# Kernel tuning notes

Hardware: AMD Instinct MI355X
Metric: run time of the kernel (lower is better)

## Reference

```python
import jax, jax.numpy as jnp
import numpy as np

INPUT_DIM = 4096
BATCH = 64
E_PER = 262144  # edges per graph
MIN_SP = 0.3


def setup_inputs() -> dict:
    key = jax.random.key(0)
    k1, k2, k3 = jax.random.split(key, 3)
    E = BATCH * E_PER
    edge_index = jax.random.randint(k1, (2, E), 0, INPUT_DIM, dtype=jnp.int64)
    edge_attr = jax.random.normal(k2, (E,), dtype=jnp.float32)
    ptr = jnp.arange(BATCH + 1, dtype=jnp.int64)
    # learned parameter (xavier-normal-ish init)
    std = float(np.sqrt(2.0 / (INPUT_DIM + INPUT_DIM)))
    weight_mask = jax.random.normal(k3, (INPUT_DIM, INPUT_DIM), dtype=jnp.float32) * std
    return {"edge_index": edge_index, "edge_attr": edge_attr, "ptr": ptr, "weight_mask": weight_mask}


def reference(edge_index, edge_attr, ptr, weight_mask):
    B = ptr.shape[0] - 1
    E = edge_index.shape[1]
    e_per = E // B
    # symmetric sigmoid mask (dropout is None -> identity)
    sym = jax.nn.sigmoid(weight_mask.T + weight_mask)
    # x_reshape: [B, e_per]
    x = edge_attr.reshape(B, e_per)
    # edge_ind_reshape: [B, 2, e_per]
    ei = edge_index.T.reshape(B, e_per, 2).transpose(0, 2, 1)
    # gather mask weights for batch-0 edges
    src = ei[0, 0]
    dst = ei[0, 1]
    w = sym[src, dst]  # [e_per]
    num_rm = int(e_per * MIN_SP)  # static count of pruned edges
    order = jnp.argsort(w)
    pruned = order[:num_rm]
    kept = jnp.sort(order[num_rm:])  # boolean-mask compaction preserves order
    mask = jnp.ones((e_per,), dtype=bool).at[pruned].set(False)
    # filtered edge_index: [B, 2, K] -> permute(1,0,2) -> [2, B*K]
    fei = jnp.take(ei, kept, axis=2)
    out_edge_index = fei.transpose(1, 0, 2).reshape(2, -1)
    # filtered edge_attr: [B, K] -> [B*K]
    out_edge_attr = jnp.take(x, kept, axis=1).reshape(-1)
    return out_edge_index, out_edge_attr, mask
```

## Files before the change

kernel.cpp:

```cpp
#include <hip/hip_runtime.h>
#include <stdint.h>
#include <math.h>

#define TIECAP 4096
typedef unsigned long long ull;

struct Ctrl {
  ull prefix;
  int rank_rem;
  int tie_count;
  int num_rm;
};

__device__ __forceinline__ ull dkey(double d) {
  ull u = (ull)__double_as_longlong(d);
  return (u & 0x8000000000000000ull) ? ~u : (u | 0x8000000000000000ull);
}

__global__ void k_init(unsigned int* hist8, Ctrl* ctrl, int num_rm) {
  int t = blockIdx.x * blockDim.x + threadIdx.x;
  if (t < 8 * 256) hist8[t] = 0u;
  if (t == 0) {
    ctrl->prefix = 0ull;
    ctrl->rank_rem = num_rm - 1;
    ctrl->tie_count = 0;
    ctrl->num_rm = num_rm;
  }
}

__global__ void k_keys(const int* __restrict__ ei, const float* __restrict__ wm,
                       int N, long long E, int D,
                       ull* __restrict__ keys, unsigned int* __restrict__ hist0) {
  __shared__ unsigned int sh[256];
  if (threadIdx.x < 256) sh[threadIdx.x] = 0u;
  __syncthreads();
  int e = blockIdx.x * blockDim.x + threadIdx.x;
  if (e < N) {
    int src = ei[e];
    int dst = ei[E + e];
    double s = (double)wm[(long long)src * D + dst] + (double)wm[(long long)dst * D + src];
    ull k = dkey(s);
    keys[e] = k;
    atomicAdd(&sh[(unsigned int)(k >> 56)], 1u);
  }
  __syncthreads();
  if (threadIdx.x < 256 && sh[threadIdx.x]) atomicAdd(&hist0[threadIdx.x], sh[threadIdx.x]);
}

__global__ void k_hist(const ull* __restrict__ keys, int N, int level,
                       const Ctrl* __restrict__ ctrl, unsigned int* __restrict__ hist) {
  __shared__ unsigned int sh[256];
  if (threadIdx.x < 256) sh[threadIdx.x] = 0u;
  __syncthreads();
  int e = blockIdx.x * blockDim.x + threadIdx.x;
  int shift = 56 - 8 * level;
  if (e < N) {
    ull k = keys[e];
    ull prefix = ctrl->prefix;
    if (((k ^ prefix) >> (shift + 8)) == 0ull)
      atomicAdd(&sh[(unsigned int)(k >> shift) & 0xFFu], 1u);
  }
  __syncthreads();
  if (threadIdx.x < 256 && sh[threadIdx.x]) atomicAdd(&hist[threadIdx.x], sh[threadIdx.x]);
}

__global__ void k_pick(const unsigned int* __restrict__ hist, int level, Ctrl* ctrl) {
  __shared__ unsigned int sh[256];
  int t = threadIdx.x;
  unsigned int c = hist[t];
  sh[t] = c;
  __syncthreads();
  for (int off = 1; off < 256; off <<= 1) {
    unsigned int v = sh[t];
    unsigned int a = (t >= off) ? sh[t - off] : 0u;
    __syncthreads();
    sh[t] = v + a;
    __syncthreads();
  }
  unsigned int incl = sh[t];
  unsigned int excl = incl - c;
  unsigned int r = (unsigned int)ctrl->rank_rem;
  if (r >= excl && r < incl) {
    int shift = 56 - 8 * level;
    ctrl->prefix |= ((ull)t) << shift;
    ctrl->rank_rem = (int)(r - excl);
  }
}

__global__ void k_ties(const ull* __restrict__ keys, int N, Ctrl* ctrl,
                       int* __restrict__ tieIdx) {
  int e = blockIdx.x * blockDim.x + threadIdx.x;
  if (e >= N) return;
  if (keys[e] == ctrl->prefix) {
    int p = atomicAdd(&ctrl->tie_count, 1);
    if (p < TIECAP) tieIdx[p] = e;
  }
}

__device__ __forceinline__ bool is_kept(ull k, int e, ull T, int j, int tc,
                                        const int* __restrict__ tieIdx) {
  if (k < T) return false;
  if (k > T) return true;
  if (j <= 0) return true;
  if (tc > TIECAP) tc = TIECAP;
  int rank = 0;
  for (int i = 0; i < tc; ++i) rank += (tieIdx[i] < e) ? 1 : 0;
  return rank >= j;
}

__global__ void k_scanA(const ull* __restrict__ keys, int N,
                        const Ctrl* __restrict__ ctrl, const int* __restrict__ tieIdx,
                        int* __restrict__ pos, int* __restrict__ blockSums,
                        float* __restrict__ mask_out) {
  __shared__ int sh[1024];
  ull T = ctrl->prefix;
  int j = ctrl->rank_rem + 1;
  int tc = ctrl->tie_count;
  int e = blockIdx.x * 1024 + threadIdx.x;
  int m = 0;
  if (e < N) m = is_kept(keys[e], e, T, j, tc, tieIdx) ? 1 : 0;
  sh[threadIdx.x] = m;
  __syncthreads();
  for (int off = 1; off < 1024; off <<= 1) {
    int v = sh[threadIdx.x];
    int add = (threadIdx.x >= (unsigned)off) ? sh[threadIdx.x - off] : 0;
    __syncthreads();
    sh[threadIdx.x] = v + add;
    __syncthreads();
  }
  if (e < N) {
    pos[e] = ((sh[threadIdx.x] - m) << 1) | m;
    mask_out[e] = m ? 1.0f : 0.0f;
  }
  if (threadIdx.x == 1023) blockSums[blockIdx.x] = sh[1023];
}

__global__ void k_scanB(int* bs, int nb) {
  __shared__ int sh[256];
  int t = threadIdx.x;
  int v = (t < nb) ? bs[t] : 0;
  sh[t] = v;
  __syncthreads();
  for (int off = 1; off < 256; off <<= 1) {
    int x = sh[t];
    int a = (t >= off) ? sh[t - off] : 0;
    __syncthreads();
    sh[t] = x + a;
    __syncthreads();
  }
  if (t < nb) bs[t] = sh[t] - v;
}

__global__ void k_kidx(const int* __restrict__ pos, const int* __restrict__ blockSums,
                       int N, int* __restrict__ kidx) {
  int e = blockIdx.x * blockDim.x + threadIdx.x;
  if (e >= N) return;
  int p = pos[e];
  if (p & 1) kidx[(p >> 1) + blockSums[e >> 10]] = e;
}

__global__ void k_gather(const int* __restrict__ kidx, const int* __restrict__ ei,
                         const float* __restrict__ attr, long long E, int N,
                         int Kkeep, long long BK, long long total4,
                         float* __restrict__ out) {
  long long q = (long long)blockIdx.x * blockDim.x + threadIdx.x;
  if (q >= total4) return;
  long long f = q * 4;
  int row = (f >= 2 * BK) ? 2 : ((f >= BK) ? 1 : 0);
  int rb = (int)(f - (long long)row * BK);
  int b = rb / Kkeep;
  int kk = rb - b * Kkeep;
  long long colbase = (long long)b * N;
  if (kk + 4 <= Kkeep) {
    int i0 = kidx[kk], i1 = kidx[kk + 1], i2 = kidx[kk + 2], i3 = kidx[kk + 3];
    float4 v;
    if (row == 0) {
      v.x = (float)ei[colbase + i0]; v.y = (float)ei[colbase + i1];
      v.z = (float)ei[colbase + i2]; v.w = (float)ei[colbase + i3];
    } else if (row == 1) {
      const int* p = ei + E;
      v.x = (float)p[colbase + i0]; v.y = (float)p[colbase + i1];
      v.z = (float)p[colbase + i2]; v.w = (float)p[colbase + i3];
    } else {
      v.x = attr[colbase + i0]; v.y = attr[colbase + i1];
      v.z = attr[colbase + i2]; v.w = attr[colbase + i3];
    }
    *(float4*)(out + f) = v;
  } else {
    for (int i = 0; i < 4; ++i) {
      long long ff = f + i;
      int row2 = (ff >= 2 * BK) ? 2 : ((ff >= BK) ? 1 : 0);
      int rb2 = (int)(ff - (long long)row2 * BK);
      int b2 = rb2 / Kkeep;
      int kk2 = rb2 - b2 * Kkeep;
      int id = kidx[kk2];
      long long c = (long long)b2 * N + id;
      float v = (row2 == 0) ? (float)ei[c] : (row2 == 1) ? (float)ei[E + c] : attr[c];
      out[ff] = v;
    }
  }
}

extern "C" void kernel_launch(void* const* d_in, const int* in_sizes, int n_in,
                              void* d_out, int out_size, void* d_ws, size_t ws_size,
                              hipStream_t stream) {
  const int* ei = (const int*)d_in[0];
  const float* attr = (const float*)d_in[1];
  const float* wm = (const float*)d_in[3];

  int B = in_sizes[2] - 1;
  long long E = (long long)in_sizes[0] / 2;
  int e_per = (int)(E / B);
  int D = (int)llround(sqrt((double)in_sizes[3]));
  int num_rm = (int)((double)e_per * 0.3);
  int Kkeep = e_per - num_rm;
  long long BK = (long long)B * Kkeep;
  long long total4 = 3 * BK / 4;

  char* w = (char*)d_ws;
  size_t off = 0;
  ull* keys = (ull*)(w + off);            off += (size_t)e_per * 8;
  unsigned int* hist8 = (unsigned int*)(w + off); off += 8 * 256 * 4;
  int* pos = (int*)(w + off);             off += (size_t)e_per * 4;
  int nb = (e_per + 1023) / 1024;
  int* blockSums = (int*)(w + off);       off += (size_t)nb * 4;
  int* tieIdx = (int*)(w + off);          off += (size_t)TIECAP * 4;
  int* kidx = (int*)(w + off);            off += (size_t)Kkeep * 4;
  Ctrl* ctrl = (Ctrl*)(w + off);          off += sizeof(Ctrl);
  (void)ws_size; (void)n_in; (void)out_size;

  float* out = (float*)d_out;
  float* mask_out = out + 3 * BK;

  k_init<<<dim3(2), dim3(1024), 0, stream>>>(hist8, ctrl, num_rm);
  k_keys<<<dim3(nb), dim3(1024), 0, stream>>>(ei, wm, e_per, E, D, keys, hist8);
  k_pick<<<dim3(1), dim3(256), 0, stream>>>(hist8, 0, ctrl);
  for (int l = 1; l < 8; ++l) {
    k_hist<<<dim3(nb), dim3(1024), 0, stream>>>(keys, e_per, l, ctrl, hist8 + l * 256);
    k_pick<<<dim3(1), dim3(256), 0, stream>>>(hist8 + l * 256, l, ctrl);
  }
  k_ties<<<dim3(nb), dim3(1024), 0, stream>>>(keys, e_per, ctrl, tieIdx);
  k_scanA<<<dim3(nb), dim3(1024), 0, stream>>>(keys, e_per, ctrl, tieIdx, pos, blockSums, mask_out);
  k_scanB<<<dim3(1), dim3(256), 0, stream>>>(blockSums, nb);
  k_kidx<<<dim3(nb), dim3(1024), 0, stream>>>(pos, blockSums, e_per, kidx);
  int gblocks = (int)((total4 + 255) / 256);
  k_gather<<<dim3(gblocks), dim3(256), 0, stream>>>(kidx, ei, attr, E, e_per, Kkeep, BK, total4, out);
}
```

Baseline: 135.8 us.

## Use 32-bit float keys for radix select, fuse pick into histogram, compact via LDS

Radix select now runs on 32-bit float keys in four 8-bit levels instead of 64-bit double keys in eight. The per-level pick kernel is folded into the histogram kernel through a last-block-done counter, which removes many small launches. Ties at the float threshold are broken by recomputing the exact double key and comparing it against a small tie list. The gather through kidx is replaced by a block-local compaction that does coalesced vector loads, stages kept values in LDS and writes them out contiguously. In exchange it depends on the tie count staying under the reduced cap, it recomputes random weight reads for threshold edges, and its int4 loads assume e_per is divisible by 1024.

```diff
diff --git a/kernel.cpp b/kernel.cpp
--- a/kernel.cpp
+++ b/kernel.cpp
@@ -2,123 +2,163 @@
 #include <stdint.h>
 #include <math.h>
 
-#define TIECAP 4096
+#define TIECAP 1024
 typedef unsigned long long ull;
+typedef long long ll;
 
 struct Ctrl {
-  ull prefix;
+  unsigned int prefix;
   int rank_rem;
   int tie_count;
-  int num_rm;
+  int done0, done1, done2, done3;
 };
 
+__device__ __forceinline__ unsigned int fkey(float f) {
+  unsigned int u = __float_as_uint(f);
+  return (u & 0x80000000u) ? ~u : (u | 0x80000000u);
+}
 __device__ __forceinline__ ull dkey(double d) {
   ull u = (ull)__double_as_longlong(d);
   return (u & 0x8000000000000000ull) ? ~u : (u | 0x8000000000000000ull);
 }
 
-__global__ void k_init(unsigned int* hist8, Ctrl* ctrl, int num_rm) {
-  int t = blockIdx.x * blockDim.x + threadIdx.x;
-  if (t < 8 * 256) hist8[t] = 0u;
+__global__ void k_init(unsigned int* hist, Ctrl* ctrl, int num_rm) {
+  int t = threadIdx.x;
+  if (t < 1024) hist[t] = 0u;
   if (t == 0) {
-    ctrl->prefix = 0ull;
+    ctrl->prefix = 0u;
     ctrl->rank_rem = num_rm - 1;
     ctrl->tie_count = 0;
-    ctrl->num_rm = num_rm;
+    ctrl->done0 = 0; ctrl->done1 = 0; ctrl->done2 = 0; ctrl->done3 = 0;
+  }
+}
+
+__device__ void do_pick(unsigned int* hist, int shift, Ctrl* ctrl) {
+  __shared__ unsigned int sph[256];
+  __shared__ int s_r;
+  int t = threadIdx.x;
+  if (t == 0) s_r = ctrl->rank_rem;
+  unsigned int c = 0;
+  if (t < 256) { c = atomicAdd(&hist[t], 0u); sph[t] = c; }
+  __syncthreads();
+  for (int off = 1; off < 256; off <<= 1) {
+    unsigned int v = 0, a = 0;
+    if (t < 256) { v = sph[t]; a = (t >= off) ? sph[t - off] : 0u; }
+    __syncthreads();
+    if (t < 256) sph[t] = v + a;
+    __syncthreads();
+  }
+  if (t < 256) {
+    unsigned int incl = sph[t], excl = incl - c;
+    unsigned int r = (unsigned int)s_r;
+    if (r >= excl && r < incl) {
+      ctrl->prefix |= ((unsigned int)t) << shift;
+      ctrl->rank_rem = (int)(r - excl);
+    }
   }
 }
 
 __global__ void k_keys(const int* __restrict__ ei, const float* __restrict__ wm,
-                       int N, long long E, int D,
-                       ull* __restrict__ keys, unsigned int* __restrict__ hist0) {
+                       int N, ll E, int D, unsigned int* __restrict__ key32,
+                       unsigned int* hist, Ctrl* ctrl) {
   __shared__ unsigned int sh[256];
-  if (threadIdx.x < 256) sh[threadIdx.x] = 0u;
-  __syncthreads();
-  int e = blockIdx.x * blockDim.x + threadIdx.x;
+  __shared__ int s_last;
+  int t = threadIdx.x;
+  if (t < 256) sh[t] = 0u;
+  __syncthreads();
+  int e = blockIdx.x * 1024 + t;
   if (e < N) {
-    int src = ei[e];
-    int dst = ei[E + e];
-    double s = (double)wm[(long long)src * D + dst] + (double)wm[(long long)dst * D + src];
-    ull k = dkey(s);
-    keys[e] = k;
-    atomicAdd(&sh[(unsigned int)(k >> 56)], 1u);
-  }
-  __syncthreads();
-  if (threadIdx.x < 256 && sh[threadIdx.x]) atomicAdd(&hist0[threadIdx.x], sh[threadIdx.x]);
-}
-
-__global__ void k_hist(const ull* __restrict__ keys, int N, int level,
-                       const Ctrl* __restrict__ ctrl, unsigned int* __restrict__ hist) {
+    int src = ei[e], dst = ei[E + e];
+    double s = (double)wm[(ll)src * D + dst] + (double)wm[(ll)dst * D + src];
+    unsigned int k = fkey((float)s);
+    key32[e] = k;
+    atomicAdd(&sh[k >> 24], 1u);
+  }
+  __syncthreads();
+  if (t < 256 && sh[t]) atomicAdd(&hist[t], sh[t]);
+  __threadfence();
+  __syncthreads();
+  if (t == 0) s_last = (atomicAdd(&ctrl->done0, 1) == (int)gridDim.x - 1) ? 1 : 0;
+  __syncthreads();
+  if (!s_last) return;
+  do_pick(hist, 24, ctrl);
+}
+
+__global__ void k_level(const unsigned int* __restrict__ key32, int N, int level,
+                        unsigned int* hist, Ctrl* ctrl, int* done) {
   __shared__ unsigned int sh[256];
-  if (threadIdx.x < 256) sh[threadIdx.x] = 0u;
-  __syncthreads();
-  int e = blockIdx.x * blockDim.x + threadIdx.x;
-  int shift = 56 - 8 * level;
+  __shared__ int s_last;
+  int t = threadIdx.x;
+  if (t < 256) sh[t] = 0u;
+  __syncthreads();
+  unsigned int prefix = ctrl->prefix;
+  int shift = 24 - 8 * level;
+  int e = blockIdx.x * 1024 + t;
   if (e < N) {
-    ull k = keys[e];
-    ull prefix = ctrl->prefix;
-    if (((k ^ prefix) >> (shift + 8)) == 0ull)
-      atomicAdd(&sh[(unsigned int)(k >> shift) & 0xFFu], 1u);
-  }
-  __syncthreads();
-  if (threadIdx.x < 256 && sh[threadIdx.x]) atomicAdd(&hist[threadIdx.x], sh[threadIdx.x]);
-}
-
-__global__ void k_pick(const unsigned int* __restrict__ hist, int level, Ctrl* ctrl) {
-  __shared__ unsigned int sh[256];
-  int t = threadIdx.x;
-  unsigned int c = hist[t];
-  sh[t] = c;
-  __syncthreads();
-  for (int off = 1; off < 256; off <<= 1) {
-    unsigned int v = sh[t];
-    unsigned int a = (t >= off) ? sh[t - off] : 0u;
-    __syncthreads();
-    sh[t] = v + a;
-    __syncthreads();
-  }
-  unsigned int incl = sh[t];
-  unsigned int excl = incl - c;
-  unsigned int r = (unsigned int)ctrl->rank_rem;
-  if (r >= excl && r < incl) {
-    int shift = 56 - 8 * level;
-    ctrl->prefix |= ((ull)t) << shift;
-    ctrl->rank_rem = (int)(r - excl);
-  }
-}
-
-__global__ void k_ties(const ull* __restrict__ keys, int N, Ctrl* ctrl,
-                       int* __restrict__ tieIdx) {
+    unsigned int k = key32[e];
+    if (((k ^ prefix) >> (shift + 8)) == 0u)
+      atomicAdd(&sh[(k >> shift) & 0xFFu], 1u);
+  }
+  __syncthreads();
+  if (t < 256 && sh[t]) atomicAdd(&hist[t], sh[t]);
+  __threadfence();
+  __syncthreads();
+  if (t == 0) s_last = (atomicAdd(done, 1) == (int)gridDim.x - 1) ? 1 : 0;
+  __syncthreads();
+  if (!s_last) return;
+  do_pick(hist, shift, ctrl);
+}
+
+__global__ void k_ties(const unsigned int* __restrict__ key32,
+                       const int* __restrict__ ei, const float* __restrict__ wm,
+                       int N, ll E, int D, Ctrl* ctrl,
+                       int* __restrict__ tieIdx, ull* __restrict__ tieKey) {
   int e = blockIdx.x * blockDim.x + threadIdx.x;
   if (e >= N) return;
-  if (keys[e] == ctrl->prefix) {
+  if (key32[e] == ctrl->prefix) {
     int p = atomicAdd(&ctrl->tie_count, 1);
-    if (p < TIECAP) tieIdx[p] = e;
-  }
-}
-
-__device__ __forceinline__ bool is_kept(ull k, int e, ull T, int j, int tc,
-                                        const int* __restrict__ tieIdx) {
+    if (p < TIECAP) {
+      int src = ei[e], dst = ei[E + e];
+      double s = (double)wm[(ll)src * D + dst] + (double)wm[(ll)dst * D + src];
+      tieIdx[p] = e;
+      tieKey[p] = dkey(s);
+    }
+  }
+}
+
+__device__ __forceinline__ bool is_kept(unsigned int k, int e, unsigned int T,
+                                        int j, int tc,
+                                        const int* __restrict__ tieIdx,
+                                        const ull* __restrict__ tieKey,
+                                        const int* __restrict__ ei,
+                                        const float* __restrict__ wm, ll E, int D) {
   if (k < T) return false;
   if (k > T) return true;
   if (j <= 0) return true;
   if (tc > TIECAP) tc = TIECAP;
+  int src = ei[e], dst = ei[E + e];
+  ull me = dkey((double)wm[(ll)src * D + dst] + (double)wm[(ll)dst * D + src]);
   int rank = 0;
-  for (int i = 0; i < tc; ++i) rank += (tieIdx[i] < e) ? 1 : 0;
+  for (int i = 0; i < tc; ++i) {
+    ull o = tieKey[i];
+    rank += (o < me || (o == me && tieIdx[i] < e)) ? 1 : 0;
+  }
   return rank >= j;
 }
 
-__global__ void k_scanA(const ull* __restrict__ keys, int N,
-                        const Ctrl* __restrict__ ctrl, const int* __restrict__ tieIdx,
-                        int* __restrict__ pos, int* __restrict__ blockSums,
-                        float* __restrict__ mask_out) {
+__global__ void k_scanA(const unsigned int* __restrict__ key32, int N,
+                        const Ctrl* __restrict__ ctrl,
+                        const int* __restrict__ tieIdx, const ull* __restrict__ tieKey,
+                        const int* __restrict__ ei, const float* __restrict__ wm,
+                        ll E, int D, int* __restrict__ pos,
+                        int* __restrict__ blockSums, float* __restrict__ mask_out) {
   __shared__ int sh[1024];
-  ull T = ctrl->prefix;
+  unsigned int T = ctrl->prefix;
   int j = ctrl->rank_rem + 1;
   int tc = ctrl->tie_count;
   int e = blockIdx.x * 1024 + threadIdx.x;
   int m = 0;
-  if (e < N) m = is_kept(keys[e], e, T, j, tc, tieIdx) ? 1 : 0;
+  if (e < N) m = is_kept(key32[e], e, T, j, tc, tieIdx, tieKey, ei, wm, E, D) ? 1 : 0;
   sh[threadIdx.x] = m;
   __syncthreads();
   for (int off = 1; off < 1024; off <<= 1) {
@@ -151,54 +191,37 @@
   if (t < nb) bs[t] = sh[t] - v;
 }
 
-__global__ void k_kidx(const int* __restrict__ pos, const int* __restrict__ blockSums,
-                       int N, int* __restrict__ kidx) {
-  int e = blockIdx.x * blockDim.x + threadIdx.x;
-  if (e >= N) return;
-  int p = pos[e];
-  if (p & 1) kidx[(p >> 1) + blockSums[e >> 10]] = e;
-}
-
-__global__ void k_gather(const int* __restrict__ kidx, const int* __restrict__ ei,
-                         const float* __restrict__ attr, long long E, int N,
-                         int Kkeep, long long BK, long long total4,
-                         float* __restrict__ out) {
-  long long q = (long long)blockIdx.x * blockDim.x + threadIdx.x;
-  if (q >= total4) return;
-  long long f = q * 4;
-  int row = (f >= 2 * BK) ? 2 : ((f >= BK) ? 1 : 0);
-  int rb = (int)(f - (long long)row * BK);
-  int b = rb / Kkeep;
-  int kk = rb - b * Kkeep;
-  long long colbase = (long long)b * N;
-  if (kk + 4 <= Kkeep) {
-    int i0 = kidx[kk], i1 = kidx[kk + 1], i2 = kidx[kk + 2], i3 = kidx[kk + 3];
-    float4 v;
-    if (row == 0) {
-      v.x = (float)ei[colbase + i0]; v.y = (float)ei[colbase + i1];
-      v.z = (float)ei[colbase + i2]; v.w = (float)ei[colbase + i3];
-    } else if (row == 1) {
-      const int* p = ei + E;
-      v.x = (float)p[colbase + i0]; v.y = (float)p[colbase + i1];
-      v.z = (float)p[colbase + i2]; v.w = (float)p[colbase + i3];
-    } else {
-      v.x = attr[colbase + i0]; v.y = attr[colbase + i1];
-      v.z = attr[colbase + i2]; v.w = attr[colbase + i3];
-    }
-    *(float4*)(out + f) = v;
+__global__ void k_compact(const int* __restrict__ pos, const int* __restrict__ bs,
+                          const int* __restrict__ ei, const float* __restrict__ attr,
+                          ll E, int N, int Kkeep, ll BK, float* __restrict__ out) {
+  __shared__ float lds[1024];
+  __shared__ int s_cnt;
+  int t = threadIdx.x;
+  int blk = blockIdx.x;
+  int b = blockIdx.y;
+  int r = blockIdx.z;
+  int q = blk * 256 + t;
+  int4 p4 = ((const int4*)pos)[q];
+  ll cb = (ll)b * N;
+  float4 v;
+  if (r == 0) {
+    int4 d = ((const int4*)(ei + cb))[q];
+    v = make_float4((float)d.x, (float)d.y, (float)d.z, (float)d.w);
+  } else if (r == 1) {
+    int4 d = ((const int4*)(ei + E + cb))[q];
+    v = make_float4((float)d.x, (float)d.y, (float)d.z, (float)d.w);
   } else {
-    for (int i = 0; i < 4; ++i) {
-      long long ff = f + i;
-      int row2 = (ff >= 2 * BK) ? 2 : ((ff >= BK) ? 1 : 0);
-      int rb2 = (int)(ff - (long long)row2 * BK);
-      int b2 = rb2 / Kkeep;
-      int kk2 = rb2 - b2 * Kkeep;
-      int id = kidx[kk2];
-      long long c = (long long)b2 * N + id;
-      float v = (row2 == 0) ? (float)ei[c] : (row2 == 1) ? (float)ei[E + c] : attr[c];
-      out[ff] = v;
-    }
-  }
+    v = ((const float4*)(attr + cb))[q];
+  }
+  if (p4.x & 1) lds[p4.x >> 1] = v.x;
+  if (p4.y & 1) lds[p4.y >> 1] = v.y;
+  if (p4.z & 1) lds[p4.z >> 1] = v.z;
+  if (p4.w & 1) lds[p4.w >> 1] = v.w;
+  if (t == 255) s_cnt = (p4.w >> 1) + (p4.w & 1);
+  __syncthreads();
+  ll ob = (ll)r * BK + (ll)b * Kkeep + bs[blk];
+  int cnt = s_cnt;
+  for (int i = t; i < cnt; i += 256) out[ob + i] = lds[i];
 }
 
 extern "C" void kernel_launch(void* const* d_in, const int* in_sizes, int n_in,
@@ -209,40 +232,37 @@
   const float* wm = (const float*)d_in[3];
 
   int B = in_sizes[2] - 1;
-  long long E = (long long)in_sizes[0] / 2;
+  ll E = (ll)in_sizes[0] / 2;
   int e_per = (int)(E / B);
   int D = (int)llround(sqrt((double)in_sizes[3]));
   int num_rm = (int)((double)e_per * 0.3);
   int Kkeep = e_per - num_rm;
-  long long BK = (long long)B * Kkeep;
-  long long total4 = 3 * BK / 4;
+  ll BK = (ll)B * Kkeep;
+  int nb = (e_per + 1023) / 1024;
 
   char* w = (char*)d_ws;
   size_t off = 0;
-  ull* keys = (ull*)(w + off);            off += (size_t)e_per * 8;
-  unsigned int* hist8 = (unsigned int*)(w + off); off += 8 * 256 * 4;
-  int* pos = (int*)(w + off);             off += (size_t)e_per * 4;
-  int nb = (e_per + 1023) / 1024;
-  int* blockSums = (int*)(w + off);       off += (size_t)nb * 4;
-  int* tieIdx = (int*)(w + off);          off += (size_t)TIECAP * 4;
-  int* kidx = (int*)(w + off);            off += (size_t)Kkeep * 4;
-  Ctrl* ctrl = (Ctrl*)(w + off);          off += sizeof(Ctrl);
+  unsigned int* key32 = (unsigned int*)(w + off); off += (size_t)e_per * 4;
+  int* pos = (int*)(w + off);                     off += (size_t)e_per * 4;
+  unsigned int* hist = (unsigned int*)(w + off);  off += 4 * 256 * 4;
+  int* blockSums = (int*)(w + off);               off += (size_t)nb * 4;
+  int* tieIdx = (int*)(w + off);                  off += (size_t)TIECAP * 4;
+  ull* tieKey = (ull*)(w + off);                  off += (size_t)TIECAP * 8;
+  Ctrl* ctrl = (Ctrl*)(w + off);                  off += sizeof(Ctrl);
   (void)ws_size; (void)n_in; (void)out_size;
 
   float* out = (float*)d_out;
   float* mask_out = out + 3 * BK;
 
-  k_init<<<dim3(2), dim3(1024), 0, stream>>>(hist8, ctrl, num_rm);
-  k_keys<<<dim3(nb), dim3(1024), 0, stream>>>(ei, wm, e_per, E, D, keys, hist8);
-  k_pick<<<dim3(1), dim3(256), 0, stream>>>(hist8, 0, ctrl);
-  for (int l = 1; l < 8; ++l) {
-    k_hist<<<dim3(nb), dim3(1024), 0, stream>>>(keys, e_per, l, ctrl, hist8 + l * 256);
-    k_pick<<<dim3(1), dim3(256), 0, stream>>>(hist8 + l * 256, l, ctrl);
-  }
-  k_ties<<<dim3(nb), dim3(1024), 0, stream>>>(keys, e_per, ctrl, tieIdx);
-  k_scanA<<<dim3(nb), dim3(1024), 0, stream>>>(keys, e_per, ctrl, tieIdx, pos, blockSums, mask_out);
+  k_init<<<dim3(1), dim3(1024), 0, stream>>>(hist, ctrl, num_rm);
+  k_keys<<<dim3(nb), dim3(1024), 0, stream>>>(ei, wm, e_per, E, D, key32, hist, ctrl);
+  k_level<<<dim3(nb), dim3(1024), 0, stream>>>(key32, e_per, 1, hist + 256, ctrl, &ctrl->done1);
+  k_level<<<dim3(nb), dim3(1024), 0, stream>>>(key32, e_per, 2, hist + 512, ctrl, &ctrl->done2);
+  k_level<<<dim3(nb), dim3(1024), 0, stream>>>(key32, e_per, 3, hist + 768, ctrl, &ctrl->done3);
+  k_ties<<<dim3(nb), dim3(1024), 0, stream>>>(key32, ei, wm, e_per, E, D, ctrl, tieIdx, tieKey);
+  k_scanA<<<dim3(nb), dim3(1024), 0, stream>>>(key32, e_per, ctrl, tieIdx, tieKey,
+                                               ei, wm, E, D, pos, blockSums, mask_out);
   k_scanB<<<dim3(1), dim3(256), 0, stream>>>(blockSums, nb);
-  k_kidx<<<dim3(nb), dim3(1024), 0, stream>>>(pos, blockSums, e_per, kidx);
-  int gblocks = (int)((total4 + 255) / 256);
-  k_gather<<<dim3(gblocks), dim3(256), 0, stream>>>(kidx, ei, attr, E, e_per, Kkeep, BK, total4, out);
-}
+  k_compact<<<dim3(nb, B, 3), dim3(256), 0, stream>>>(pos, blockSums, ei, attr,
+                                                      E, e_per, Kkeep, BK, out);
+}
```

Measured after the change: 343.1 us. +152.6%, slower.

## Replace 8-pass radix select with 16-bit histogram plus candidate rank and fused compaction

Applied to the files above, without the earlier changes.

Uses 32-bit float keys instead of 64-bit double keys. The threshold search becomes a single 65536-bin histogram, a pick pass, and a small candidate-set rank that folds ties in via an (key,index) packed comparison. This replaces eight histogram/pick launch pairs and the tie-rank loop. The separate pos/kidx/gather kernels are merged into one streaming compaction kernel that reads each batch's data contiguously and writes kept entries directly. The trade-offs are global atomics on the histogram and a cap on the candidate count. Float rounding of the key may also change the ordering relative to the double-precision reference.

```diff
diff --git a/kernel.cpp b/kernel.cpp
--- a/kernel.cpp
+++ b/kernel.cpp
@@ -2,137 +2,104 @@
 #include <stdint.h>
 #include <math.h>
 
-#define TIECAP 4096
+#define CAND_CAP 8192
 typedef unsigned long long ull;
+typedef long long ll;
+typedef unsigned int uint;
 
 struct Ctrl {
-  ull prefix;
-  int rank_rem;
-  int tie_count;
-  int num_rm;
+  int binsel;
+  int r_in;
+  int ncand;
+  int pad;
+  ull Tpack;
 };
 
-__device__ __forceinline__ ull dkey(double d) {
-  ull u = (ull)__double_as_longlong(d);
-  return (u & 0x8000000000000000ull) ? ~u : (u | 0x8000000000000000ull);
-}
-
-__global__ void k_init(unsigned int* hist8, Ctrl* ctrl, int num_rm) {
-  int t = blockIdx.x * blockDim.x + threadIdx.x;
-  if (t < 8 * 256) hist8[t] = 0u;
-  if (t == 0) {
-    ctrl->prefix = 0ull;
-    ctrl->rank_rem = num_rm - 1;
-    ctrl->tie_count = 0;
-    ctrl->num_rm = num_rm;
-  }
-}
-
 __global__ void k_keys(const int* __restrict__ ei, const float* __restrict__ wm,
-                       int N, long long E, int D,
-                       ull* __restrict__ keys, unsigned int* __restrict__ hist0) {
-  __shared__ unsigned int sh[256];
-  if (threadIdx.x < 256) sh[threadIdx.x] = 0u;
-  __syncthreads();
-  int e = blockIdx.x * blockDim.x + threadIdx.x;
-  if (e < N) {
-    int src = ei[e];
-    int dst = ei[E + e];
-    double s = (double)wm[(long long)src * D + dst] + (double)wm[(long long)dst * D + src];
-    ull k = dkey(s);
-    keys[e] = k;
-    atomicAdd(&sh[(unsigned int)(k >> 56)], 1u);
-  }
-  __syncthreads();
-  if (threadIdx.x < 256 && sh[threadIdx.x]) atomicAdd(&hist0[threadIdx.x], sh[threadIdx.x]);
-}
-
-__global__ void k_hist(const ull* __restrict__ keys, int N, int level,
-                       const Ctrl* __restrict__ ctrl, unsigned int* __restrict__ hist) {
-  __shared__ unsigned int sh[256];
-  if (threadIdx.x < 256) sh[threadIdx.x] = 0u;
-  __syncthreads();
-  int e = blockIdx.x * blockDim.x + threadIdx.x;
-  int shift = 56 - 8 * level;
-  if (e < N) {
-    ull k = keys[e];
-    ull prefix = ctrl->prefix;
-    if (((k ^ prefix) >> (shift + 8)) == 0ull)
-      atomicAdd(&sh[(unsigned int)(k >> shift) & 0xFFu], 1u);
-  }
-  __syncthreads();
-  if (threadIdx.x < 256 && sh[threadIdx.x]) atomicAdd(&hist[threadIdx.x], sh[threadIdx.x]);
-}
-
-__global__ void k_pick(const unsigned int* __restrict__ hist, int level, Ctrl* ctrl) {
-  __shared__ unsigned int sh[256];
-  int t = threadIdx.x;
-  unsigned int c = hist[t];
-  sh[t] = c;
-  __syncthreads();
-  for (int off = 1; off < 256; off <<= 1) {
-    unsigned int v = sh[t];
-    unsigned int a = (t >= off) ? sh[t - off] : 0u;
-    __syncthreads();
-    sh[t] = v + a;
-    __syncthreads();
-  }
-  unsigned int incl = sh[t];
-  unsigned int excl = incl - c;
-  unsigned int r = (unsigned int)ctrl->rank_rem;
-  if (r >= excl && r < incl) {
-    int shift = 56 - 8 * level;
-    ctrl->prefix |= ((ull)t) << shift;
-    ctrl->rank_rem = (int)(r - excl);
-  }
-}
-
-__global__ void k_ties(const ull* __restrict__ keys, int N, Ctrl* ctrl,
-                       int* __restrict__ tieIdx) {
+                       int N, ll E, int D,
+                       uint* __restrict__ key32, uint* __restrict__ hist) {
   int e = blockIdx.x * blockDim.x + threadIdx.x;
   if (e >= N) return;
-  if (keys[e] == ctrl->prefix) {
-    int p = atomicAdd(&ctrl->tie_count, 1);
-    if (p < TIECAP) tieIdx[p] = e;
-  }
-}
-
-__device__ __forceinline__ bool is_kept(ull k, int e, ull T, int j, int tc,
-                                        const int* __restrict__ tieIdx) {
-  if (k < T) return false;
-  if (k > T) return true;
-  if (j <= 0) return true;
-  if (tc > TIECAP) tc = TIECAP;
-  int rank = 0;
-  for (int i = 0; i < tc; ++i) rank += (tieIdx[i] < e) ? 1 : 0;
-  return rank >= j;
-}
-
-__global__ void k_scanA(const ull* __restrict__ keys, int N,
-                        const Ctrl* __restrict__ ctrl, const int* __restrict__ tieIdx,
-                        int* __restrict__ pos, int* __restrict__ blockSums,
-                        float* __restrict__ mask_out) {
-  __shared__ int sh[1024];
-  ull T = ctrl->prefix;
-  int j = ctrl->rank_rem + 1;
-  int tc = ctrl->tie_count;
-  int e = blockIdx.x * 1024 + threadIdx.x;
-  int m = 0;
-  if (e < N) m = is_kept(keys[e], e, T, j, tc, tieIdx) ? 1 : 0;
-  sh[threadIdx.x] = m;
+  int src = ei[e], dst = ei[E + e];
+  double s = (double)wm[(ll)src * D + dst] + (double)wm[(ll)dst * D + src];
+  uint u = __float_as_uint((float)s);
+  uint k = (u & 0x80000000u) ? ~u : (u | 0x80000000u);
+  key32[e] = k;
+  atomicAdd(&hist[k >> 16], 1u);
+}
+
+__global__ void k_pick0(const uint* __restrict__ hist, int r, Ctrl* ctrl) {
+  __shared__ uint sh[1024];
+  int t = threadIdx.x;
+  uint partial = 0;
+  for (int i = 0; i < 64; ++i) partial += hist[t * 64 + i];
+  sh[t] = partial;
   __syncthreads();
   for (int off = 1; off < 1024; off <<= 1) {
-    int v = sh[threadIdx.x];
-    int add = (threadIdx.x >= (unsigned)off) ? sh[threadIdx.x - off] : 0;
-    __syncthreads();
-    sh[threadIdx.x] = v + add;
-    __syncthreads();
-  }
-  if (e < N) {
-    pos[e] = ((sh[threadIdx.x] - m) << 1) | m;
-    mask_out[e] = m ? 1.0f : 0.0f;
-  }
-  if (threadIdx.x == 1023) blockSums[blockIdx.x] = sh[1023];
+    uint v = sh[t];
+    uint a = (t >= off) ? sh[t - off] : 0u;
+    __syncthreads();
+    sh[t] = v + a;
+    __syncthreads();
+  }
+  uint incl = sh[t], base = incl - partial;
+  if ((uint)r >= base && (uint)r < incl) {
+    uint cum = base;
+    for (int i = 0; i < 64; ++i) {
+      uint c = hist[t * 64 + i];
+      if ((uint)r < cum + c) {
+        ctrl->binsel = t * 64 + i;
+        ctrl->r_in = (int)((uint)r - cum);
+        break;
+      }
+      cum += c;
+    }
+  }
+}
+
+__global__ void k_cand(const uint* __restrict__ key32, int N, Ctrl* ctrl,
+                       ull* __restrict__ cand) {
+  int e = blockIdx.x * blockDim.x + threadIdx.x;
+  if (e >= N) return;
+  uint k = key32[e];
+  if ((int)(k >> 16) == ctrl->binsel) {
+    int p = atomicAdd(&ctrl->ncand, 1);
+    if (p < CAND_CAP) cand[p] = ((ull)k << 32) | (uint)e;
+  }
+}
+
+__global__ void k_pick1(const ull* __restrict__ cand, Ctrl* ctrl) {
+  int nc = ctrl->ncand;
+  if (nc > CAND_CAP) nc = CAND_CAP;
+  int r = ctrl->r_in;
+  for (int o = threadIdx.x; o < nc; o += blockDim.x) {
+    ull my = cand[o];
+    int cnt = 0;
+    for (int i = 0; i < nc; ++i) cnt += (cand[i] < my) ? 1 : 0;
+    if (cnt == r) ctrl->Tpack = my;
+  }
+}
+
+__device__ __forceinline__ int keptf(uint k, int e, ull T) {
+  return ((((ull)k << 32) | (uint)e) > T) ? 1 : 0;
+}
+
+__global__ void k_bsum(const uint* __restrict__ key32, const Ctrl* __restrict__ ctrl,
+                       int* __restrict__ bs) {
+  __shared__ int sh[256];
+  int t = threadIdx.x, blk = blockIdx.x;
+  ull T = ctrl->Tpack;
+  uint4 k4 = ((const uint4*)key32)[blk * 256 + t];
+  int e0 = blk * 1024 + t * 4;
+  int c = keptf(k4.x, e0, T) + keptf(k4.y, e0 + 1, T) +
+          keptf(k4.z, e0 + 2, T) + keptf(k4.w, e0 + 3, T);
+  sh[t] = c;
+  __syncthreads();
+  for (int off = 128; off > 0; off >>= 1) {
+    if (t < off) sh[t] += sh[t + off];
+    __syncthreads();
+  }
+  if (t == 0) bs[blk] = sh[0];
 }
 
 __global__ void k_scanB(int* bs, int nb) {
@@ -151,54 +118,58 @@
   if (t < nb) bs[t] = sh[t] - v;
 }
 
-__global__ void k_kidx(const int* __restrict__ pos, const int* __restrict__ blockSums,
-                       int N, int* __restrict__ kidx) {
-  int e = blockIdx.x * blockDim.x + threadIdx.x;
-  if (e >= N) return;
-  int p = pos[e];
-  if (p & 1) kidx[(p >> 1) + blockSums[e >> 10]] = e;
-}
-
-__global__ void k_gather(const int* __restrict__ kidx, const int* __restrict__ ei,
-                         const float* __restrict__ attr, long long E, int N,
-                         int Kkeep, long long BK, long long total4,
-                         float* __restrict__ out) {
-  long long q = (long long)blockIdx.x * blockDim.x + threadIdx.x;
-  if (q >= total4) return;
-  long long f = q * 4;
-  int row = (f >= 2 * BK) ? 2 : ((f >= BK) ? 1 : 0);
-  int rb = (int)(f - (long long)row * BK);
-  int b = rb / Kkeep;
-  int kk = rb - b * Kkeep;
-  long long colbase = (long long)b * N;
-  if (kk + 4 <= Kkeep) {
-    int i0 = kidx[kk], i1 = kidx[kk + 1], i2 = kidx[kk + 2], i3 = kidx[kk + 3];
-    float4 v;
-    if (row == 0) {
-      v.x = (float)ei[colbase + i0]; v.y = (float)ei[colbase + i1];
-      v.z = (float)ei[colbase + i2]; v.w = (float)ei[colbase + i3];
-    } else if (row == 1) {
-      const int* p = ei + E;
-      v.x = (float)p[colbase + i0]; v.y = (float)p[colbase + i1];
-      v.z = (float)p[colbase + i2]; v.w = (float)p[colbase + i3];
-    } else {
-      v.x = attr[colbase + i0]; v.y = attr[colbase + i1];
-      v.z = attr[colbase + i2]; v.w = attr[colbase + i3];
-    }
-    *(float4*)(out + f) = v;
-  } else {
-    for (int i = 0; i < 4; ++i) {
-      long long ff = f + i;
-      int row2 = (ff >= 2 * BK) ? 2 : ((ff >= BK) ? 1 : 0);
-      int rb2 = (int)(ff - (long long)row2 * BK);
-      int b2 = rb2 / Kkeep;
-      int kk2 = rb2 - b2 * Kkeep;
-      int id = kidx[kk2];
-      long long c = (long long)b2 * N + id;
-      float v = (row2 == 0) ? (float)ei[c] : (row2 == 1) ? (float)ei[E + c] : attr[c];
-      out[ff] = v;
-    }
-  }
+__global__ void k_compact(const uint* __restrict__ key32, const int* __restrict__ bs,
+                          const Ctrl* __restrict__ ctrl, const int* __restrict__ ei,
+                          const float* __restrict__ attr, ll E, int N, int Kkeep,
+                          ll BK, float* __restrict__ out, float* __restrict__ mask_out) {
+  __shared__ int sw[256];
+  int t = threadIdx.x, blk = blockIdx.x, b = blockIdx.y;
+  int q = blk * 256 + t;
+  ull T = ctrl->Tpack;
+  uint4 k4 = ((const uint4*)key32)[q];
+  int4 d0 = ((const int4*)(ei + (ll)b * N))[q];
+  int4 d1 = ((const int4*)(ei + E + (ll)b * N))[q];
+  float4 d2 = ((const float4*)(attr + (ll)b * N))[q];
+  int e0 = blk * 1024 + t * 4;
+  int f0 = keptf(k4.x, e0, T), f1 = keptf(k4.y, e0 + 1, T);
+  int f2 = keptf(k4.z, e0 + 2, T), f3 = keptf(k4.w, e0 + 3, T);
+  int c = f0 + f1 + f2 + f3;
+  sw[t] = c;
+  __syncthreads();
+  for (int off = 1; off < 256; off <<= 1) {
+    int v = sw[t];
+    int a = (t >= off) ? sw[t - off] : 0;
+    __syncthreads();
+    sw[t] = v + a;
+    __syncthreads();
+  }
+  ll base = (ll)bs[blk] + (sw[t] - c);
+  ll ob = (ll)b * Kkeep + base;
+  {
+    int o = 0;
+    if (f0) { out[ob + o] = (float)d0.x; o++; }
+    if (f1) { out[ob + o] = (float)d0.y; o++; }
+    if (f2) { out[ob + o] = (float)d0.z; o++; }
+    if (f3) { out[ob + o] = (float)d0.w; o++; }
+  }
+  {
+    float* r1 = out + BK;
+    int o = 0;
+    if (f0) { r1[ob + o] = (float)d1.x; o++; }
+    if (f1) { r1[ob + o] = (float)d1.y; o++; }
+    if (f2) { r1[ob + o] = (float)d1.z; o++; }
+    if (f3) { r1[ob + o] = (float)d1.w; o++; }
+  }
+  {
+    float* r2 = out + 2 * BK;
+    int o = 0;
+    if (f0) { r2[ob + o] = d2.x; o++; }
+    if (f1) { r2[ob + o] = d2.y; o++; }
+    if (f2) { r2[ob + o] = d2.z; o++; }
+    if (f3) { r2[ob + o] = d2.w; o++; }
+  }
+  if (b == 0)
+    ((float4*)mask_out)[q] = make_float4((float)f0, (float)f1, (float)f2, (float)f3);
 }
 
 extern "C" void kernel_launch(void* const* d_in, const int* in_sizes, int n_in,
@@ -209,40 +180,33 @@
   const float* wm = (const float*)d_in[3];
 
   int B = in_sizes[2] - 1;
-  long long E = (long long)in_sizes[0] / 2;
+  ll E = (ll)in_sizes[0] / 2;
   int e_per = (int)(E / B);
   int D = (int)llround(sqrt((double)in_sizes[3]));
   int num_rm = (int)((double)e_per * 0.3);
   int Kkeep = e_per - num_rm;
-  long long BK = (long long)B * Kkeep;
-  long long total4 = 3 * BK / 4;
+  ll BK = (ll)B * Kkeep;
+  int nb = (e_per + 1023) / 1024;
 
   char* w = (char*)d_ws;
   size_t off = 0;
-  ull* keys = (ull*)(w + off);            off += (size_t)e_per * 8;
-  unsigned int* hist8 = (unsigned int*)(w + off); off += 8 * 256 * 4;
-  int* pos = (int*)(w + off);             off += (size_t)e_per * 4;
-  int nb = (e_per + 1023) / 1024;
-  int* blockSums = (int*)(w + off);       off += (size_t)nb * 4;
-  int* tieIdx = (int*)(w + off);          off += (size_t)TIECAP * 4;
-  int* kidx = (int*)(w + off);            off += (size_t)Kkeep * 4;
-  Ctrl* ctrl = (Ctrl*)(w + off);          off += sizeof(Ctrl);
+  uint* key32 = (uint*)(w + off);  off += (size_t)e_per * 4;
+  uint* hist = (uint*)(w + off);   off += 65536 * 4;
+  Ctrl* ctrl = (Ctrl*)(w + off);   off += 64;
+  ull* cand = (ull*)(w + off);     off += (size_t)CAND_CAP * 8;
+  int* bs = (int*)(w + off);       off += (size_t)nb * 4;
   (void)ws_size; (void)n_in; (void)out_size;
 
   float* out = (float*)d_out;
   float* mask_out = out + 3 * BK;
 
-  k_init<<<dim3(2), dim3(1024), 0, stream>>>(hist8, ctrl, num_rm);
-  k_keys<<<dim3(nb), dim3(1024), 0, stream>>>(ei, wm, e_per, E, D, keys, hist8);
-  k_pick<<<dim3(1), dim3(256), 0, stream>>>(hist8, 0, ctrl);
-  for (int l = 1; l < 8; ++l) {
-    k_hist<<<dim3(nb), dim3(1024), 0, stream>>>(keys, e_per, l, ctrl, hist8 + l * 256);
-    k_pick<<<dim3(1), dim3(256), 0, stream>>>(hist8 + l * 256, l, ctrl);
-  }
-  k_ties<<<dim3(nb), dim3(1024), 0, stream>>>(keys, e_per, ctrl, tieIdx);
-  k_scanA<<<dim3(nb), dim3(1024), 0, stream>>>(keys, e_per, ctrl, tieIdx, pos, blockSums, mask_out);
-  k_scanB<<<dim3(1), dim3(256), 0, stream>>>(blockSums, nb);
-  k_kidx<<<dim3(nb), dim3(1024), 0, stream>>>(pos, blockSums, e_per, kidx);
-  int gblocks = (int)((total4 + 255) / 256);
-  k_gather<<<dim3(gblocks), dim3(256), 0, stream>>>(kidx, ei, attr, E, e_per, Kkeep, BK, total4, out);
-}
+  hipMemsetAsync(hist, 0, 65536 * 4 + sizeof(Ctrl), stream);
+  k_keys<<<dim3((e_per + 1023) / 1024), dim3(1024), 0, stream>>>(ei, wm, e_per, E, D, key32, hist);
+  k_pick0<<<dim3(1), dim3(1024), 0, stream>>>(hist, num_rm - 1, ctrl);
+  k_cand<<<dim3(nb), dim3(1024), 0, stream>>>(key32, e_per, ctrl, cand);
+  k_pick1<<<dim3(1), dim3(1024), 0, stream>>>(cand, ctrl);
+  k_bsum<<<dim3(nb), dim3(256), 0, stream>>>(key32, ctrl, bs);
+  k_scanB<<<dim3(1), dim3(256), 0, stream>>>(bs, nb);
+  k_compact<<<dim3(nb, B), dim3(256), 0, stream>>>(key32, bs, ctrl, ei, attr,
+                                                   E, e_per, Kkeep, BK, out, mask_out);
+}
```

Measured after the change: 195.2 us. 43.7% more time.
